# Kernel optimization log

Hardware: AMD Instinct MI355X
Metric: run time of the kernel (lower is better)

## Reference

```python
import jax, jax.numpy as jnp
import numpy as np

B, C, L, D, E, K = 64, 23, 26000, 64, 512, 3  # batch, chromosomes, bins/chr, d_model, eos_dim, num_states
V = C * L


def setup_inputs() -> dict:
    key = jax.random.key(0)
    k0, k1, k2, k3 = jax.random.split(key, 4)
    return {
        "eos_emb": jax.random.normal(k0, (B, C, E), jnp.float32),
        "bin_ids": jnp.arange(C * L, dtype=jnp.int32).reshape(C, L),
        "emb_table": jax.random.normal(k1, (V, D), jnp.float32) * 0.02,
        "eos_W": jax.random.normal(k2, (D, E), jnp.float32) / np.float32(np.sqrt(E)),
        "eos_b": jnp.zeros((D,), jnp.float32),
        "fc_W": jax.random.normal(k3, (K, 2 * D), jnp.float32) / np.float32(np.sqrt(2 * D)),
        "fc_b": jnp.zeros((K,), jnp.float32),
    }


def reference(eos_emb, bin_ids, emb_table, eos_W, eos_b, fc_W, fc_b):
    # eos_projection (use_eos_proj=True): [B,C,E] @ [D,E]^T + b -> [B,C,D]
    eos = jnp.einsum('bce,de->bcd', eos_emb, eos_W) + eos_b
    # per-chromosome embedding gather (bin_projection skipped: bin_emb_dim == d_model, use_bin_proj=False)
    bin_emb = emb_table[bin_ids]  # [C,L,D]
    # fc on concat([bin, eos]) == bin @ Wb^T + eos @ We^T + b (avoids materializing [B,C,L,2D])
    Wb, We = fc_W[:, :D], fc_W[:, D:]
    a = jnp.einsum('cld,kd->clk', bin_emb, Wb)          # [C,L,K]
    e = jnp.einsum('bcd,kd->bck', eos, We) + fc_b       # [B,C,K]
    return jax.nn.relu(a[None, :, :, :] + e[:, :, None, :])  # [B,C,L,K]
```

## Files before the change

### kernel.cpp

```cpp
#include <hip/hip_runtime.h>

#define NB 64
#define NC 23
#define NL 26000
#define ND 64
#define NE 512
#define NK 3
#define FP4  (NL * NK / 4)
#define CFP4 (NC * FP4)
#define CHUNK 3504
#define NCHUNK 128
#define NJ 14
#define GB 8

typedef float v4f __attribute__((ext_vector_type(4)));

__global__ __launch_bounds__(256) void eos_e_kernel(
    const float* __restrict__ eos_emb,
    const float* __restrict__ eos_W,
    const float* __restrict__ eos_b,
    const float* __restrict__ fc_W,
    const float* __restrict__ fc_b,
    float* __restrict__ e_out)
{
    const int bc = blockIdx.x;
    const int t  = threadIdx.x;
    const int q  = t & 3;
    const int d  = t >> 2;

    __shared__ v4f xs4[NE / 4];
    if (t < NE / 4)
        xs4[t] = reinterpret_cast<const v4f*>(eos_emb + (size_t)bc * NE)[t];
    __syncthreads();

    const v4f* wrow = reinterpret_cast<const v4f*>(eos_W + (size_t)d * NE);
    v4f acc = (v4f)(0.f);
    #pragma unroll 8
    for (int j = 0; j < NE / 16; ++j) {
        const int idx = q + 4 * j;
        acc += wrow[idx] * xs4[idx];
    }
    float p = (acc.x + acc.y) + (acc.z + acc.w);
    p += __shfl_xor(p, 1, 64);
    p += __shfl_xor(p, 2, 64);
    const float eosd = p + eos_b[d];

    __shared__ float part[4][NK];
    #pragma unroll
    for (int k = 0; k < NK; ++k) {
        float pk = eosd * fc_W[k * (2 * ND) + ND + d];
        pk += __shfl_xor(pk,  4, 64);
        pk += __shfl_xor(pk,  8, 64);
        pk += __shfl_xor(pk, 16, 64);
        pk += __shfl_xor(pk, 32, 64);
        if ((t & 63) == 0) part[t >> 6][k] = pk;
    }
    __syncthreads();
    if (t < NK)
        e_out[(size_t)bc * NK + t] =
            part[0][t] + part[1][t] + part[2][t] + part[3][t] + fc_b[t];
}

__global__ __launch_bounds__(256) void a_kernel(
    const int*   __restrict__ bin_ids,
    const float* __restrict__ emb_table,
    const float* __restrict__ fc_W,
    float* __restrict__ a_out)
{
    const int c = blockIdx.y;
    const int t = threadIdx.x;
    const int q = t & 3;
    const int r = t >> 2;
    const int l = blockIdx.x * 64 + r;

    __shared__ v4f wb4[NK][ND / 4];
    if (t < NK * (ND / 4)) {
        const int k = t / (ND / 4), i = t % (ND / 4);
        wb4[k][i] = reinterpret_cast<const v4f*>(fc_W + (size_t)k * (2 * ND))[i];
    }
    __syncthreads();
    if (l >= NL) return;

    const int row = bin_ids[(size_t)c * NL + l];
    const v4f* er = reinterpret_cast<const v4f*>(emb_table + (size_t)row * ND);

    v4f s0 = (v4f)(0.f), s1 = (v4f)(0.f), s2 = (v4f)(0.f);
    #pragma unroll
    for (int j = 0; j < 4; ++j) {
        const int idx = q + 4 * j;
        const v4f v = er[idx];
        s0 += v * wb4[0][idx];
        s1 += v * wb4[1][idx];
        s2 += v * wb4[2][idx];
    }
    float a0 = (s0.x + s0.y) + (s0.z + s0.w);
    float a1 = (s1.x + s1.y) + (s1.z + s1.w);
    float a2 = (s2.x + s2.y) + (s2.z + s2.w);
    a0 += __shfl_xor(a0, 1, 64); a0 += __shfl_xor(a0, 2, 64);
    a1 += __shfl_xor(a1, 1, 64); a1 += __shfl_xor(a1, 2, 64);
    a2 += __shfl_xor(a2, 1, 64); a2 += __shfl_xor(a2, 2, 64);

    if (q < NK) {
        const float val = (q == 0) ? a0 : (q == 1) ? a1 : a2;
        a_out[((size_t)c * NL + l) * NK + q] = val;
    }
}

__global__ __launch_bounds__(256) void bstream_kernel(
    const float* __restrict__ a_in,
    const float* __restrict__ e_in,
    float* __restrict__ out)
{
    const int bx = blockIdx.x;
    const int b0 = blockIdx.y * GB;
    const int t  = threadIdx.x;

    __shared__ v4f e4[3][NC][GB];
    for (int i = t; i < 3 * NC * GB; i += 256) {
        const int p   = i / (NC * GB);
        const int rem = i - p * (NC * GB);
        const int c   = rem / GB;
        const int bl  = rem - c * GB;
        const float* ep = e_in + ((size_t)(b0 + bl) * NC + c) * NK;
        const float e0 = ep[0], e1 = ep[1], e2 = ep[2];
        v4f v;
        if      (p == 0) { v.x = e0; v.y = e1; v.z = e2; v.w = e0; }
        else if (p == 1) { v.x = e1; v.y = e2; v.z = e0; v.w = e1; }
        else             { v.x = e2; v.y = e0; v.z = e1; v.w = e2; }
        e4[p][c][bl] = v;
    }
    __syncthreads();

    const int base = bx * CHUNK;
    const v4f* a4 = reinterpret_cast<const v4f*>(a_in);

    v4f        av[NJ];
    const v4f* eptr[NJ];
    bool       gj[NJ];
    #pragma unroll
    for (int j = 0; j < NJ; ++j) {
        const int fo = j * 256 + t;
        const int f  = base + fo;
        gj[j] = (fo < CHUNK) && (f < CFP4);
        const int fc = gj[j] ? f : 0;
        const int p  = fc % 3;
        const int c  = fc / FP4;
        eptr[j] = &e4[p][c][0];
        av[j]   = gj[j] ? a4[fc] : (v4f)(0.f);
    }

    v4f* o4 = reinterpret_cast<v4f*>(out);
    size_t obase = (size_t)b0 * CFP4 + base;
    #pragma unroll 2
    for (int bl = 0; bl < GB; ++bl) {
        #pragma unroll
        for (int j = 0; j < NJ; ++j) {
            if (gj[j]) {
                const v4f ev = eptr[j][bl];
                v4f o;
                o.x = fmaxf(av[j].x + ev.x, 0.f);
                o.y = fmaxf(av[j].y + ev.y, 0.f);
                o.z = fmaxf(av[j].z + ev.z, 0.f);
                o.w = fmaxf(av[j].w + ev.w, 0.f);
                o4[obase + j * 256 + t] = o;
            }
        }
        obase += CFP4;
    }
}

__global__ __launch_bounds__(256) void decoder_fused_kernel(
    const int*   __restrict__ bin_ids,
    const float* __restrict__ emb_table,
    const float* __restrict__ fc_W,
    const float* __restrict__ e_in,
    float* __restrict__ out)
{
    const int c   = blockIdx.y;
    const int tid = threadIdx.x;
    const int l   = blockIdx.x * 256 + tid;

    __shared__ float wb[NK][ND];
    __shared__ float es[NB * NK];

    if (tid < NK * ND)
        wb[tid / ND][tid % ND] = fc_W[(tid / ND) * (2 * ND) + (tid % ND)];
    if (tid < NB * NK) {
        int b = tid / NK, k = tid % NK;
        es[tid] = e_in[((size_t)b * NC + c) * NK + k];
    }
    __syncthreads();
    if (l >= NL) return;

    const int row = bin_ids[(size_t)c * NL + l];
    const float4* er = reinterpret_cast<const float4*>(emb_table + (size_t)row * ND);
    const float4* w0 = reinterpret_cast<const float4*>(wb[0]);
    const float4* w1 = reinterpret_cast<const float4*>(wb[1]);
    const float4* w2 = reinterpret_cast<const float4*>(wb[2]);

    float a0 = 0.f, a1 = 0.f, a2 = 0.f;
    #pragma unroll
    for (int i = 0; i < ND / 4; ++i) {
        float4 v  = er[i];
        float4 p0 = w0[i], p1 = w1[i], p2 = w2[i];
        a0 += v.x * p0.x + v.y * p0.y + v.z * p0.z + v.w * p0.w;
        a1 += v.x * p1.x + v.y * p1.y + v.z * p1.z + v.w * p1.w;
        a2 += v.x * p2.x + v.y * p2.y + v.z * p2.z + v.w * p2.w;
    }

    size_t obase = ((size_t)c * NL + l) * NK;
    const size_t bstride = (size_t)NC * NL * NK;
    #pragma unroll 4
    for (int b = 0; b < NB; ++b) {
        const float e0 = es[b * NK + 0];
        const float e1 = es[b * NK + 1];
        const float e2 = es[b * NK + 2];
        out[obase + 0] = fmaxf(a0 + e0, 0.f);
        out[obase + 1] = fmaxf(a1 + e1, 0.f);
        out[obase + 2] = fmaxf(a2 + e2, 0.f);
        obase += bstride;
    }
}

extern "C" void kernel_launch(void* const* d_in, const int* in_sizes, int n_in,
                              void* d_out, int out_size, void* d_ws, size_t ws_size,
                              hipStream_t stream) {
    const float* eos_emb   = (const float*)d_in[0];
    const int*   bin_ids   = (const int*)  d_in[1];
    const float* emb_table = (const float*)d_in[2];
    const float* eos_W     = (const float*)d_in[3];
    const float* eos_b     = (const float*)d_in[4];
    const float* fc_W      = (const float*)d_in[5];
    const float* fc_b      = (const float*)d_in[6];
    float*       out       = (float*)d_out;

    float*  e_ws = (float*)d_ws;
    const size_t a_off_bytes = 32768;
    float*  a_ws = (float*)((char*)d_ws + a_off_bytes);
    const size_t a_bytes = (size_t)NC * NL * NK * sizeof(float);

    eos_e_kernel<<<NB * NC, 256, 0, stream>>>(eos_emb, eos_W, eos_b, fc_W, fc_b, e_ws);

    if (ws_size >= a_off_bytes + a_bytes) {
        dim3 grid_a((NL + 63) / 64, NC);
        a_kernel<<<grid_a, 256, 0, stream>>>(bin_ids, emb_table, fc_W, a_ws);

        dim3 grid_b(NCHUNK, NB / GB);
        bstream_kernel<<<grid_b, 256, 0, stream>>>(a_ws, e_ws, out);
    } else {
        dim3 grid((NL + 255) / 256, NC);
        decoder_fused_kernel<<<grid, 256, 0, stream>>>(bin_ids, emb_table, fc_W, e_ws, out);
    }
}
```

Baseline: 146.6 us.

## Fuse bin projection into broadcast kernel with LDS staging and nontemporal stores

Merges the a_kernel and bstream_kernel into one kernel. Each block computes its span of the per-bin projections into LDS, then broadcasts them across all 64 batches, writing the output with nontemporal stores. This drops the global round trip of the intermediate a buffer and one kernel launch. In exchange each block loops over all batches, with at most two float4 outputs per thread per batch, and handles at most two chromosomes per chunk through per-chunk e tables.

```diff
diff --git a/kernel.cpp b/kernel.cpp
--- a/kernel.cpp
+++ b/kernel.cpp
@@ -6,12 +6,11 @@
 #define ND 64
 #define NE 512
 #define NK 3
-#define FP4  (NL * NK / 4)
-#define CFP4 (NC * FP4)
-#define CHUNK 3504
-#define NCHUNK 128
-#define NJ 14
-#define GB 8
+#define FP4   (NL * NK / 4)
+#define CFP4  (NC * FP4)
+#define CHUNK 438
+#define NCHUNK 1024
+#define GLSPAN 584
 
 typedef float v4f __attribute__((ext_vector_type(4)));
 
@@ -61,111 +60,119 @@
             part[0][t] + part[1][t] + part[2][t] + part[3][t] + fc_b[t];
 }
 
-__global__ __launch_bounds__(256) void a_kernel(
+__global__ __launch_bounds__(256) void fused_kernel(
     const int*   __restrict__ bin_ids,
     const float* __restrict__ emb_table,
     const float* __restrict__ fc_W,
-    float* __restrict__ a_out)
+    const float* __restrict__ e_in,
+    float* __restrict__ out)
 {
-    const int c = blockIdx.y;
-    const int t = threadIdx.x;
-    const int q = t & 3;
-    const int r = t >> 2;
-    const int l = blockIdx.x * 64 + r;
-
-    __shared__ v4f wb4[NK][ND / 4];
+    const int bx    = blockIdx.x;
+    const int t     = threadIdx.x;
+    const int base  = bx * CHUNK;
+    const int gl_lo = bx * GLSPAN;
+
+    __shared__ v4f   wb4[NK][ND / 4];
+    __shared__ v4f   e4[3][NB][2];
+    __shared__ float a_lds[GLSPAN * 3];
+
+    const int c_lo = base / FP4;
+    const int c_hi_raw = (base + CHUNK - 1) / FP4;
+    const int c_hi = (c_hi_raw < NC) ? c_hi_raw : (NC - 1);
+
     if (t < NK * (ND / 4)) {
         const int k = t / (ND / 4), i = t % (ND / 4);
         wb4[k][i] = reinterpret_cast<const v4f*>(fc_W + (size_t)k * (2 * ND))[i];
     }
-    __syncthreads();
-    if (l >= NL) return;
-
-    const int row = bin_ids[(size_t)c * NL + l];
-    const v4f* er = reinterpret_cast<const v4f*>(emb_table + (size_t)row * ND);
-
-    v4f s0 = (v4f)(0.f), s1 = (v4f)(0.f), s2 = (v4f)(0.f);
+    {
+        const int i = t;
+        for (int it = i; it < 3 * NB * 2; it += 256) {
+            const int p   = it / (NB * 2);
+            const int rem = it - p * (NB * 2);
+            const int bl  = rem >> 1;
+            const int ci  = rem & 1;
+            const int c   = ci ? c_hi : c_lo;
+            const float* ep = e_in + ((size_t)bl * NC + c) * NK;
+            const float e0 = ep[0], e1 = ep[1], e2 = ep[2];
+            v4f v;
+            if      (p == 0) { v.x = e0; v.y = e1; v.z = e2; v.w = e0; }
+            else if (p == 1) { v.x = e1; v.y = e2; v.z = e0; v.w = e1; }
+            else             { v.x = e2; v.y = e0; v.z = e1; v.w = e2; }
+            e4[p][bl][ci] = v;
+        }
+    }
+    __syncthreads();
+
+    const int q = t & 3;
+    const int r = t >> 2;
     #pragma unroll
-    for (int j = 0; j < 4; ++j) {
-        const int idx = q + 4 * j;
-        const v4f v = er[idx];
-        s0 += v * wb4[0][idx];
-        s1 += v * wb4[1][idx];
-        s2 += v * wb4[2][idx];
-    }
-    float a0 = (s0.x + s0.y) + (s0.z + s0.w);
-    float a1 = (s1.x + s1.y) + (s1.z + s1.w);
-    float a2 = (s2.x + s2.y) + (s2.z + s2.w);
-    a0 += __shfl_xor(a0, 1, 64); a0 += __shfl_xor(a0, 2, 64);
-    a1 += __shfl_xor(a1, 1, 64); a1 += __shfl_xor(a1, 2, 64);
-    a2 += __shfl_xor(a2, 1, 64); a2 += __shfl_xor(a2, 2, 64);
-
-    if (q < NK) {
-        const float val = (q == 0) ? a0 : (q == 1) ? a1 : a2;
-        a_out[((size_t)c * NL + l) * NK + q] = val;
-    }
-}
-
-__global__ __launch_bounds__(256) void bstream_kernel(
-    const float* __restrict__ a_in,
-    const float* __restrict__ e_in,
-    float* __restrict__ out)
-{
-    const int bx = blockIdx.x;
-    const int b0 = blockIdx.y * GB;
-    const int t  = threadIdx.x;
-
-    __shared__ v4f e4[3][NC][GB];
-    for (int i = t; i < 3 * NC * GB; i += 256) {
-        const int p   = i / (NC * GB);
-        const int rem = i - p * (NC * GB);
-        const int c   = rem / GB;
-        const int bl  = rem - c * GB;
-        const float* ep = e_in + ((size_t)(b0 + bl) * NC + c) * NK;
-        const float e0 = ep[0], e1 = ep[1], e2 = ep[2];
-        v4f v;
-        if      (p == 0) { v.x = e0; v.y = e1; v.z = e2; v.w = e0; }
-        else if (p == 1) { v.x = e1; v.y = e2; v.z = e0; v.w = e1; }
-        else             { v.x = e2; v.y = e0; v.z = e1; v.w = e2; }
-        e4[p][c][bl] = v;
-    }
-    __syncthreads();
-
-    const int base = bx * CHUNK;
-    const v4f* a4 = reinterpret_cast<const v4f*>(a_in);
-
-    v4f        av[NJ];
-    const v4f* eptr[NJ];
-    bool       gj[NJ];
-    #pragma unroll
-    for (int j = 0; j < NJ; ++j) {
-        const int fo = j * 256 + t;
-        const int f  = base + fo;
-        gj[j] = (fo < CHUNK) && (f < CFP4);
-        const int fc = gj[j] ? f : 0;
-        const int p  = fc % 3;
-        const int c  = fc / FP4;
-        eptr[j] = &e4[p][c][0];
-        av[j]   = gj[j] ? a4[fc] : (v4f)(0.f);
-    }
+    for (int pass = 0; pass < 10; ++pass) {
+        const int rl = pass * 64 + r;
+        const int gl = gl_lo + rl;
+        if (rl < GLSPAN && gl < NC * NL) {
+            const int row = bin_ids[gl];
+            const v4f* er = reinterpret_cast<const v4f*>(emb_table + (size_t)row * ND);
+            v4f s0 = (v4f)(0.f), s1 = (v4f)(0.f), s2 = (v4f)(0.f);
+            #pragma unroll
+            for (int j = 0; j < 4; ++j) {
+                const int idx = q + 4 * j;
+                const v4f v = er[idx];
+                s0 += v * wb4[0][idx];
+                s1 += v * wb4[1][idx];
+                s2 += v * wb4[2][idx];
+            }
+            float a0 = (s0.x + s0.y) + (s0.z + s0.w);
+            float a1 = (s1.x + s1.y) + (s1.z + s1.w);
+            float a2 = (s2.x + s2.y) + (s2.z + s2.w);
+            a0 += __shfl_xor(a0, 1, 64); a0 += __shfl_xor(a0, 2, 64);
+            a1 += __shfl_xor(a1, 1, 64); a1 += __shfl_xor(a1, 2, 64);
+            a2 += __shfl_xor(a2, 1, 64); a2 += __shfl_xor(a2, 2, 64);
+            if (q < NK) {
+                const float val = (q == 0) ? a0 : (q == 1) ? a1 : a2;
+                a_lds[rl * 3 + q] = val;
+            }
+        }
+    }
+    __syncthreads();
+
+    const int f0 = base + t;
+    const int p0 = f0 % 3;
+    const int ci0 = ((f0 / FP4) == c_lo) ? 0 : 1;
+    const bool v0 = (f0 < CFP4);
+    v4f a0v = (v4f)(0.f);
+    if (v0) a0v = *reinterpret_cast<const v4f*>(&a_lds[t * 4]);
+
+    const int t1 = 256 + t;
+    const bool has1 = (t1 < CHUNK);
+    const int f1 = base + t1;
+    const int p1 = has1 ? (f1 % 3) : 0;
+    const int ci1 = (has1 && (f1 / FP4) == c_lo) ? 0 : 1;
+    const bool v1 = has1 && (f1 < CFP4);
+    v4f a1v = (v4f)(0.f);
+    if (v1) a1v = *reinterpret_cast<const v4f*>(&a_lds[t1 * 4]);
 
     v4f* o4 = reinterpret_cast<v4f*>(out);
-    size_t obase = (size_t)b0 * CFP4 + base;
-    #pragma unroll 2
-    for (int bl = 0; bl < GB; ++bl) {
-        #pragma unroll
-        for (int j = 0; j < NJ; ++j) {
-            if (gj[j]) {
-                const v4f ev = eptr[j][bl];
-                v4f o;
-                o.x = fmaxf(av[j].x + ev.x, 0.f);
-                o.y = fmaxf(av[j].y + ev.y, 0.f);
-                o.z = fmaxf(av[j].z + ev.z, 0.f);
-                o.w = fmaxf(av[j].w + ev.w, 0.f);
-                o4[obase + j * 256 + t] = o;
-            }
-        }
-        obase += CFP4;
+    #pragma unroll 4
+    for (int bl = 0; bl < NB; ++bl) {
+        const size_t ob = (size_t)bl * CFP4;
+        if (v0) {
+            const v4f ev = e4[p0][bl][ci0];
+            v4f o;
+            o.x = fmaxf(a0v.x + ev.x, 0.f);
+            o.y = fmaxf(a0v.y + ev.y, 0.f);
+            o.z = fmaxf(a0v.z + ev.z, 0.f);
+            o.w = fmaxf(a0v.w + ev.w, 0.f);
+            __builtin_nontemporal_store(o, &o4[ob + f0]);
+        }
+        if (v1) {
+            const v4f ev = e4[p1][bl][ci1];
+            v4f o;
+            o.x = fmaxf(a1v.x + ev.x, 0.f);
+            o.y = fmaxf(a1v.y + ev.y, 0.f);
+            o.z = fmaxf(a1v.z + ev.z, 0.f);
+            o.w = fmaxf(a1v.w + ev.w, 0.f);
+            __builtin_nontemporal_store(o, &o4[ob + f1]);
+        }
     }
 }
 
@@ -234,19 +241,12 @@
     const float* fc_b      = (const float*)d_in[6];
     float*       out       = (float*)d_out;
 
-    float*  e_ws = (float*)d_ws;
-    const size_t a_off_bytes = 32768;
-    float*  a_ws = (float*)((char*)d_ws + a_off_bytes);
-    const size_t a_bytes = (size_t)NC * NL * NK * sizeof(float);
+    float* e_ws = (float*)d_ws;
 
     eos_e_kernel<<<NB * NC, 256, 0, stream>>>(eos_emb, eos_W, eos_b, fc_W, fc_b, e_ws);
 
-    if (ws_size >= a_off_bytes + a_bytes) {
-        dim3 grid_a((NL + 63) / 64, NC);
-        a_kernel<<<grid_a, 256, 0, stream>>>(bin_ids, emb_table, fc_W, a_ws);
-
-        dim3 grid_b(NCHUNK, NB / GB);
-        bstream_kernel<<<grid_b, 256, 0, stream>>>(a_ws, e_ws, out);
+    if (ws_size >= (size_t)NB * NC * NK * sizeof(float)) {
+        fused_kernel<<<NCHUNK, 256, 0, stream>>>(bin_ids, emb_table, fc_W, e_ws, out);
     } else {
         dim3 grid((NL + 255) / 256, NC);
         decoder_fused_kernel<<<grid, 256, 0, stream>>>(bin_ids, emb_table, fc_W, e_ws, out);
```

New measurement: 153.3 us. 1.05x slower.

## Replace batch-grouped broadcast kernel with one block per batch and chunk

Applied to the files above, without the earlier changes.

The output-writing kernel previously let each block load one chunk of `a` into registers and write it for 8 batches. It now launches one block per (batch, chunk) pair. Each block reloads its slice of `a` and looks up at most two chromosome `e` values from a tiny shared table. This gives 8x more blocks, smaller per-block setup and fewer live registers, at the cost of reading `a` 64 times instead of 8, which is meant to be served from L2.

```diff
diff --git a/kernel.cpp b/kernel.cpp
--- a/kernel.cpp
+++ b/kernel.cpp
@@ -6,12 +6,11 @@
 #define ND 64
 #define NE 512
 #define NK 3
-#define FP4  (NL * NK / 4)
-#define CFP4 (NC * FP4)
+#define FP4   (NL * NK / 4)
+#define CFP4  (NC * FP4)
 #define CHUNK 3504
 #define NCHUNK 128
 #define NJ 14
-#define GB 8
 
 typedef float v4f __attribute__((ext_vector_type(4)));
 
@@ -106,66 +105,52 @@
     }
 }
 
-__global__ __launch_bounds__(256) void bstream_kernel(
+__global__ __launch_bounds__(256) void bcopy_kernel(
     const float* __restrict__ a_in,
     const float* __restrict__ e_in,
     float* __restrict__ out)
 {
-    const int bx = blockIdx.x;
-    const int b0 = blockIdx.y * GB;
-    const int t  = threadIdx.x;
-
-    __shared__ v4f e4[3][NC][GB];
-    for (int i = t; i < 3 * NC * GB; i += 256) {
-        const int p   = i / (NC * GB);
-        const int rem = i - p * (NC * GB);
-        const int c   = rem / GB;
-        const int bl  = rem - c * GB;
-        const float* ep = e_in + ((size_t)(b0 + bl) * NC + c) * NK;
+    const int b    = blockIdx.x;
+    const int cx   = blockIdx.y;
+    const int t    = threadIdx.x;
+    const int base = cx * CHUNK;
+
+    const int c_lo = base / FP4;
+    const int c_hi_raw = (base + CHUNK - 1) / FP4;
+    const int c_hi = (c_hi_raw < NC) ? c_hi_raw : (NC - 1);
+    const int c_split = (c_lo + 1) * FP4;
+
+    __shared__ v4f e4[3][2];
+    if (t < 6) {
+        const int p = t >> 1, ci = t & 1;
+        const int c = ci ? c_hi : c_lo;
+        const float* ep = e_in + ((size_t)b * NC + c) * NK;
         const float e0 = ep[0], e1 = ep[1], e2 = ep[2];
         v4f v;
         if      (p == 0) { v.x = e0; v.y = e1; v.z = e2; v.w = e0; }
         else if (p == 1) { v.x = e1; v.y = e2; v.z = e0; v.w = e1; }
         else             { v.x = e2; v.y = e0; v.z = e1; v.w = e2; }
-        e4[p][c][bl] = v;
-    }
-    __syncthreads();
-
-    const int base = bx * CHUNK;
+        e4[p][ci] = v;
+    }
+    __syncthreads();
+
     const v4f* a4 = reinterpret_cast<const v4f*>(a_in);
-
-    v4f        av[NJ];
-    const v4f* eptr[NJ];
-    bool       gj[NJ];
+    v4f* o4 = reinterpret_cast<v4f*>(out) + (size_t)b * CFP4;
+
     #pragma unroll
     for (int j = 0; j < NJ; ++j) {
         const int fo = j * 256 + t;
         const int f  = base + fo;
-        gj[j] = (fo < CHUNK) && (f < CFP4);
-        const int fc = gj[j] ? f : 0;
-        const int p  = fc % 3;
-        const int c  = fc / FP4;
-        eptr[j] = &e4[p][c][0];
-        av[j]   = gj[j] ? a4[fc] : (v4f)(0.f);
-    }
-
-    v4f* o4 = reinterpret_cast<v4f*>(out);
-    size_t obase = (size_t)b0 * CFP4 + base;
-    #pragma unroll 2
-    for (int bl = 0; bl < GB; ++bl) {
-        #pragma unroll
-        for (int j = 0; j < NJ; ++j) {
-            if (gj[j]) {
-                const v4f ev = eptr[j][bl];
-                v4f o;
-                o.x = fmaxf(av[j].x + ev.x, 0.f);
-                o.y = fmaxf(av[j].y + ev.y, 0.f);
-                o.z = fmaxf(av[j].z + ev.z, 0.f);
-                o.w = fmaxf(av[j].w + ev.w, 0.f);
-                o4[obase + j * 256 + t] = o;
-            }
+        if (fo < CHUNK && f < CFP4) {
+            const v4f av = a4[f];
+            const v4f ev = e4[f % 3][(f >= c_split) ? 1 : 0];
+            v4f o;
+            o.x = fmaxf(av.x + ev.x, 0.f);
+            o.y = fmaxf(av.y + ev.y, 0.f);
+            o.z = fmaxf(av.z + ev.z, 0.f);
+            o.w = fmaxf(av.w + ev.w, 0.f);
+            o4[f] = o;
         }
-        obase += CFP4;
     }
 }
 
@@ -245,8 +230,8 @@
         dim3 grid_a((NL + 63) / 64, NC);
         a_kernel<<<grid_a, 256, 0, stream>>>(bin_ids, emb_table, fc_W, a_ws);
 
-        dim3 grid_b(NCHUNK, NB / GB);
-        bstream_kernel<<<grid_b, 256, 0, stream>>>(a_ws, e_ws, out);
+        dim3 grid_b(NB, NCHUNK);
+        bcopy_kernel<<<grid_b, 256, 0, stream>>>(a_ws, e_ws, out);
     } else {
         dim3 grid((NL + 255) / 256, NC);
         decoder_fused_kernel<<<grid, 256, 0, stream>>>(bin_ids, emb_table, fc_W, e_ws, out);
```

Result: slower. 167.2 us (+14.0%).
